# Kernel optimization log

Measured on AMD Instinct MI355X. Metric: run time of the kernel, lower is better.

Reference implementation:

```python
import jax, jax.numpy as jnp
import numpy as np

N_NODES = 50000
N_EDGES = 800000
N_GRAPHS = 256
IN_DIM = 64
HID = 128


def setup_inputs() -> dict:
    key = jax.random.key(0)
    ks = jax.random.split(key, 16)
    x = jax.random.normal(ks[0], (N_NODES, IN_DIM), dtype=jnp.float32)
    edge_index = jax.random.randint(ks[1], (2, N_EDGES), 0, N_NODES)
    batch = jnp.sort(jax.random.randint(ks[2], (N_NODES,), 0, N_GRAPHS))
    edge_attr = jax.random.uniform(ks[3], (N_EDGES,), dtype=jnp.float32)

    def lin(k, out_d, in_d):
        s = 1.0 / np.sqrt(in_d)
        return jax.random.uniform(k, (out_d, in_d), minval=-s, maxval=s, dtype=jnp.float32)

    params = {
        'W1r': lin(ks[4], HID, IN_DIM), 'b1': jnp.zeros((HID,), jnp.float32), 'W1root': lin(ks[5], HID, IN_DIM),
        'W2r': lin(ks[6], HID, HID), 'b2': jnp.zeros((HID,), jnp.float32), 'W2root': lin(ks[7], HID, HID),
        'W3r': lin(ks[8], HID // 2, HID), 'b3': jnp.zeros((HID // 2,), jnp.float32), 'W3root': lin(ks[9], HID // 2, HID),
        'Wm1': lin(ks[10], HID // 4, HID // 2), 'bm1': jnp.zeros((HID // 4,), jnp.float32),
        'Wm2': lin(ks[11], HID // 8, HID // 4), 'bm2': jnp.zeros((HID // 8,), jnp.float32),
        'Wm3': lin(ks[12], 1, HID // 8), 'bm3': jnp.zeros((1,), jnp.float32),
    }
    return dict(x=x, edge_index=edge_index, batch=batch, edge_attr=edge_attr, **params)


def _graph_conv(x, src, dst, ew, Wr, br, Wroot):
    # PyG GraphConv(aggr='add'): lin_rel(scatter_add(x[src]*w)) + lin_root(x)
    msg = x[src] * ew[:, None]                      # [E, d] gather + scale
    agg = jax.ops.segment_sum(msg, dst, num_segments=x.shape[0])  # [N, d]
    return agg @ Wr.T + br + x @ Wroot.T


def reference(x, edge_index, batch, edge_attr,
              W1r, b1, W1root, W2r, b2, W2root, W3r, b3, W3root,
              Wm1, bm1, Wm2, bm2, Wm3, bm3):
    src, dst = edge_index[0], edge_index[1]
    # eval mode: dropouts are identity
    h = jnp.tanh(_graph_conv(x, src, dst, edge_attr, W1r, b1, W1root))
    h = jnp.tanh(_graph_conv(h, src, dst, edge_attr, W2r, b2, W2root))
    h = jnp.tanh(_graph_conv(h, src, dst, edge_attr, W3r, b3, W3root))
    # global add pool over graphs
    g = jax.ops.segment_sum(h, batch, num_segments=N_GRAPHS)      # [G, hid//2]
    g = jax.nn.relu(g @ Wm1.T + bm1)
    g = jax.nn.relu(g @ Wm2.T + bm2)
    return g @ Wm3.T + bm3                                        # [G, 1]
```

## Files before the change

### kernel.cpp

```cpp
#include <hip/hip_runtime.h>

#define N_NODES 50000
#define N_EDGES 800000
#define N_GRAPHS 256
#define SCAN_B ((N_NODES + 255) / 256)
#define FILL_GROUPS 8
#define NPG (N_NODES / FILL_GROUPS)

typedef __attribute__((ext_vector_type(8))) short bf16x8;
typedef __attribute__((ext_vector_type(4))) float f32x4;

__device__ inline unsigned short f2bf(float f) {
    unsigned int u = __float_as_uint(f);
    u += 0x7fff + ((u >> 16) & 1);
    return (unsigned short)(u >> 16);
}
__device__ inline float bf2f(unsigned short h) {
    return __uint_as_float(((unsigned int)h) << 16);
}
__device__ inline float fast_tanh(float x) {
    return 1.0f - 2.0f / (__expf(2.0f * x) + 1.0f);
}

__global__ void pack_w_kernel(const float* __restrict__ s0, const float* __restrict__ s1,
                              int K0, int KTOT, int nconcat,
                              unsigned short* __restrict__ hi, unsigned short* __restrict__ lo)
{
    const int idx = blockIdx.x * 256 + threadIdx.x;
    if (idx >= 128 * KTOT) return;
    const int c = idx / KTOT, k = idx % KTOT;
    float v;
    if (nconcat) v = (c < 64) ? s0[c * KTOT + k] : s1[(c - 64) * KTOT + k];
    else         v = (k < K0) ? s0[c * K0 + k]   : s1[c * K0 + (k - K0)];
    const unsigned short h = f2bf(v);
    hi[idx] = h;
    lo[idx] = f2bf(v - bf2f(h));
}

template<int KTOT, bool KSPLIT, bool NBIAS, bool ACT>
__global__ __launch_bounds__(256)
void gemm_mfma(const float* __restrict__ A0, const float* __restrict__ A1, int astr,
               const unsigned short* __restrict__ Bhi, const unsigned short* __restrict__ Blo,
               const float* __restrict__ bias, float* __restrict__ C)
{
    __shared__ __align__(16) unsigned short lah[64 * 40];
    __shared__ __align__(16) unsigned short lal[64 * 40];
    __shared__ __align__(16) unsigned short lbh[128 * 40];
    __shared__ __align__(16) unsigned short lbl[128 * 40];

    const int tid = threadIdx.x;
    const int w = tid >> 6;
    const int lane = tid & 63;
    const int lrow = lane & 15;
    const int lkb = lane >> 4;
    const int m0 = blockIdx.x * 64;

    constexpr int NCH = KTOT / 32;
    f32x4 acc[4][2] = {};

    for (int ch = 0; ch < NCH; ++ch) {
        const float* __restrict__ Asel;
        int ak0;
        if (KSPLIT) {
            Asel = (ch < NCH / 2) ? A0 : A1;
            ak0 = (ch % (NCH / 2)) * 32;
        } else { Asel = A0; ak0 = ch * 32; }
        const int bk0 = ch * 32;

        __syncthreads();
#pragma unroll
        for (int p = 0; p < 2; ++p) {
            const int f = tid + p * 256;
            const int r = f >> 3;
            const int q = f & 7;
            int row = m0 + r; if (row >= N_NODES) row = N_NODES - 1;
            const float4 v = *(const float4*)&Asel[(long)row * astr + ak0 + q * 4];
            const unsigned short h0 = f2bf(v.x), h1 = f2bf(v.y), h2 = f2bf(v.z), h3 = f2bf(v.w);
            *(ushort4*)&lah[r * 40 + q * 4] = make_ushort4(h0, h1, h2, h3);
            *(ushort4*)&lal[r * 40 + q * 4] =
                make_ushort4(f2bf(v.x - bf2f(h0)), f2bf(v.y - bf2f(h1)),
                             f2bf(v.z - bf2f(h2)), f2bf(v.w - bf2f(h3)));
        }
#pragma unroll
        for (int p = 0; p < 2; ++p) {
            const int f = tid + p * 256;
            const int r = f >> 2;
            const int q = f & 3;
            const long g = (long)r * KTOT + bk0 + q * 8;
            *(uint4*)&lbh[r * 40 + q * 8] = *(const uint4*)&Bhi[g];
            *(uint4*)&lbl[r * 40 + q * 8] = *(const uint4*)&Blo[g];
        }
        __syncthreads();

        const int bo0 = (w * 32 + lrow) * 40 + lkb * 8;
        const int bo1 = bo0 + 16 * 40;
        const bf16x8 bh0 = *(const bf16x8*)&lbh[bo0];
        const bf16x8 bh1 = *(const bf16x8*)&lbh[bo1];
        const bf16x8 bl0 = *(const bf16x8*)&lbl[bo0];
        const bf16x8 bl1 = *(const bf16x8*)&lbl[bo1];
#pragma unroll
        for (int m = 0; m < 4; ++m) {
            const int ao = (m * 16 + lrow) * 40 + lkb * 8;
            const bf16x8 ah = *(const bf16x8*)&lah[ao];
            const bf16x8 al = *(const bf16x8*)&lal[ao];
            acc[m][0] = __builtin_amdgcn_mfma_f32_16x16x32_bf16(ah, bh0, acc[m][0], 0, 0, 0);
            acc[m][1] = __builtin_amdgcn_mfma_f32_16x16x32_bf16(ah, bh1, acc[m][1], 0, 0, 0);
            acc[m][0] = __builtin_amdgcn_mfma_f32_16x16x32_bf16(al, bh0, acc[m][0], 0, 0, 0);
            acc[m][1] = __builtin_amdgcn_mfma_f32_16x16x32_bf16(al, bh1, acc[m][1], 0, 0, 0);
            acc[m][0] = __builtin_amdgcn_mfma_f32_16x16x32_bf16(ah, bl0, acc[m][0], 0, 0, 0);
            acc[m][1] = __builtin_amdgcn_mfma_f32_16x16x32_bf16(ah, bl1, acc[m][1], 0, 0, 0);
        }
    }

    const int c0 = w * 32 + lrow;
    float bb0, bb1;
    if (NBIAS) {
        bb0 = (c0 < 64) ? 0.f : bias[c0 - 64];
        bb1 = (c0 + 16 < 64) ? 0.f : bias[c0 + 16 - 64];
    } else { bb0 = bias[c0]; bb1 = bias[c0 + 16]; }
#pragma unroll
    for (int m = 0; m < 4; ++m) {
#pragma unroll
        for (int r = 0; r < 4; ++r) {
            const int row = m0 + m * 16 + lkb * 4 + r;
            if (row < N_NODES) {
                const float v0 = acc[m][0][r] + bb0;
                const float v1 = acc[m][1][r] + bb1;
                C[(long)row * 128 + c0]      = ACT ? fast_tanh(v0) : v0;
                C[(long)row * 128 + c0 + 16] = ACT ? fast_tanh(v1) : v1;
            }
        }
    }
}

__global__ void count_kernel(const int* __restrict__ ei, int* __restrict__ count)
{
    const int e = blockIdx.x * blockDim.x + threadIdx.x;
    if (e < N_EDGES) atomicAdd(&count[ei[N_EDGES + e]], 1);
}

__global__ __launch_bounds__(256)
void scan_blocks_kernel(const int* __restrict__ count, int* __restrict__ blocksum)
{
    __shared__ int red[256];
    const int i = blockIdx.x * 256 + threadIdx.x;
    red[threadIdx.x] = (i < N_NODES) ? count[i] : 0;
    __syncthreads();
#pragma unroll
    for (int d = 128; d > 0; d >>= 1) {
        if (threadIdx.x < d) red[threadIdx.x] += red[threadIdx.x + d];
        __syncthreads();
    }
    if (threadIdx.x == 0) blocksum[blockIdx.x] = red[0];
}

__global__ __launch_bounds__(256)
void scan_base_kernel(const int* __restrict__ blocksum, int* __restrict__ blockbase)
{
    __shared__ int s[256];
    const int t = threadIdx.x;
    const int own = (t < SCAN_B) ? blocksum[t] : 0;
    s[t] = own;
    __syncthreads();
#pragma unroll
    for (int d = 1; d < 256; d <<= 1) {
        const int v = (t >= d) ? s[t - d] : 0;
        __syncthreads();
        s[t] += v;
        __syncthreads();
    }
    if (t < SCAN_B) blockbase[t] = s[t] - own;
}

__global__ __launch_bounds__(256)
void scan_final_kernel(const int* __restrict__ count, const int* __restrict__ blockbase,
                       int* __restrict__ offsets, int* __restrict__ cursor)
{
    __shared__ int s[256];
    const int t = threadIdx.x;
    const int i = blockIdx.x * 256 + t;
    const int v = (i < N_NODES) ? count[i] : 0;
    s[t] = v;
    __syncthreads();
#pragma unroll
    for (int d = 1; d < 256; d <<= 1) {
        const int u = (t >= d) ? s[t - d] : 0;
        __syncthreads();
        s[t] += u;
        __syncthreads();
    }
    if (i < N_NODES) {
        const int off = blockbase[blockIdx.x] + s[t] - v;
        offsets[i] = off;
        cursor[i] = off;
    }
    if (i == 0) offsets[N_NODES] = N_EDGES;
}

__global__ __launch_bounds__(256)
void fill_kernel(const int* __restrict__ ei, const float* __restrict__ ew,
                 int* __restrict__ cursor, uint2* __restrict__ rec)
{
    const int g = blockIdx.x & (FILL_GROUPS - 1);
    const int q = blockIdx.x >> 3;
    const int nlo = g * NPG;
    const int nhi = nlo + NPG;
    const int stride = (gridDim.x >> 3) * 256;
    for (int e = q * 256 + threadIdx.x; e < N_EDGES; e += stride) {
        const int t = ei[N_EDGES + e];
        if (t >= nlo && t < nhi) {
            const int pos = atomicAdd(&cursor[t], 1);
            rec[pos] = make_uint2((unsigned)ei[e], __float_as_uint(ew[e]));
        }
    }
}

template<int D>
__global__ __launch_bounds__(256)
void gather_agg(const float* __restrict__ feat, int stride,
                const int* __restrict__ offsets, const uint2* __restrict__ rec,
                float* __restrict__ agg)
{
    constexpr int LPN = D / 4;
    constexpr int NPB = 256 / LPN;
    const int lane = threadIdx.x % LPN;
    const int slot = threadIdx.x / LPN;
    const int n = blockIdx.x * NPB + slot;
    if (n >= N_NODES) return;
    const int lo = offsets[n], hi = offsets[n + 1];
    const int j = lane * 4;
    float4 a0 = make_float4(0.f, 0.f, 0.f, 0.f);
    float4 a1 = make_float4(0.f, 0.f, 0.f, 0.f);
    int e = lo;
    for (; e + 1 < hi; e += 2) {
        const uint2 r0 = rec[e];
        const uint2 r1 = rec[e + 1];
        const float4 v0 = *(const float4*)&feat[(long)r0.x * stride + j];
        const float4 v1 = *(const float4*)&feat[(long)r1.x * stride + j];
        const float w0 = __uint_as_float(r0.y);
        const float w1 = __uint_as_float(r1.y);
        a0.x = fmaf(v0.x, w0, a0.x); a0.y = fmaf(v0.y, w0, a0.y);
        a0.z = fmaf(v0.z, w0, a0.z); a0.w = fmaf(v0.w, w0, a0.w);
        a1.x = fmaf(v1.x, w1, a1.x); a1.y = fmaf(v1.y, w1, a1.y);
        a1.z = fmaf(v1.z, w1, a1.z); a1.w = fmaf(v1.w, w1, a1.w);
    }
    if (e < hi) {
        const uint2 r = rec[e];
        const float4 v = *(const float4*)&feat[(long)r.x * stride + j];
        const float w = __uint_as_float(r.y);
        a0.x = fmaf(v.x, w, a0.x); a0.y = fmaf(v.y, w, a0.y);
        a0.z = fmaf(v.z, w, a0.z); a0.w = fmaf(v.w, w, a0.w);
    }
    *(float4*)&agg[(long)n * D + j] =
        make_float4(a0.x + a1.x, a0.y + a1.y, a0.z + a1.z, a0.w + a1.w);
}

__global__ void gstart_kernel(const int* __restrict__ batch, int* __restrict__ gstart)
{
    const int g = threadIdx.x;
    int lo = 0, hi = N_NODES;
    while (lo < hi) { const int mid = (lo + hi) >> 1; if (batch[mid] < g) lo = mid + 1; else hi = mid; }
    gstart[g] = lo;
    if (g == 0) gstart[N_GRAPHS] = N_NODES;
}

__global__ __launch_bounds__(256)
void pool_seg_kernel(const float* __restrict__ agg3, const float* __restrict__ yr,
                     const int* __restrict__ gstart, float* __restrict__ g)
{
    const int gi = blockIdx.x;
    const int c = threadIdx.x & 63;
    const int sub = threadIdx.x >> 6;
    const int lo = gstart[gi], hi = gstart[gi + 1];
    float acc = 0.f;
    for (int n = lo + sub; n < hi; n += 4)
        acc += fast_tanh(agg3[(long)n * 64 + c] + yr[(long)n * 128 + 64 + c]);
    __shared__ float red[256];
    red[threadIdx.x] = acc;
    __syncthreads();
    if (sub == 0) g[gi * 64 + c] = red[c] + red[64 + c] + red[128 + c] + red[192 + c];
}

__global__ __launch_bounds__(64)
void mlp_kernel(const float* __restrict__ g,
                const float* __restrict__ Wm1, const float* __restrict__ bm1,
                const float* __restrict__ Wm2, const float* __restrict__ bm2,
                const float* __restrict__ Wm3, const float* __restrict__ bm3,
                float* __restrict__ out)
{
    const int gi = blockIdx.x;
    const int l = threadIdx.x;
    __shared__ float gr[64], h1[32], h2[16];
    gr[l] = g[gi * 64 + l];
    __syncthreads();
    if (l < 32) {
        float a = bm1[l];
        const float* w = Wm1 + l * 64;
        for (int k = 0; k < 64; ++k) a = fmaf(gr[k], w[k], a);
        h1[l] = fmaxf(a, 0.f);
    }
    __syncthreads();
    if (l < 16) {
        float a = bm2[l];
        const float* w = Wm2 + l * 32;
        for (int k = 0; k < 32; ++k) a = fmaf(h1[k], w[k], a);
        h2[l] = fmaxf(a, 0.f);
    }
    __syncthreads();
    if (l == 0) {
        float a = bm3[0];
        for (int k = 0; k < 16; ++k) a = fmaf(h2[k], Wm3[k], a);
        out[gi] = a;
    }
}

extern "C" void kernel_launch(void* const* d_in, const int* in_sizes, int n_in,
                              void* d_out, int out_size, void* d_ws, size_t ws_size,
                              hipStream_t stream) {
    const float* x      = (const float*)d_in[0];
    const int*   ei     = (const int*)  d_in[1];
    const int*   batch  = (const int*)  d_in[2];
    const float* ew     = (const float*)d_in[3];
    const float* W1r    = (const float*)d_in[4];
    const float* b1     = (const float*)d_in[5];
    const float* W1root = (const float*)d_in[6];
    const float* W2r    = (const float*)d_in[7];
    const float* b2     = (const float*)d_in[8];
    const float* W2root = (const float*)d_in[9];
    const float* W3r    = (const float*)d_in[10];
    const float* b3     = (const float*)d_in[11];
    const float* W3root = (const float*)d_in[12];
    const float* Wm1    = (const float*)d_in[13];
    const float* bm1    = (const float*)d_in[14];
    const float* Wm2    = (const float*)d_in[15];
    const float* bm2    = (const float*)d_in[16];
    const float* Wm3    = (const float*)d_in[17];
    const float* bm3    = (const float*)d_in[18];
    float* out = (float*)d_out;

    float* P0   = (float*)d_ws;
    float* P1   = P0 + (long)N_NODES * 128;
    float* P2   = P1 + (long)N_NODES * 128;
    float* POOL = P2 + (long)N_NODES * 128;
    int*   count    = (int*)(POOL + N_GRAPHS * 64);
    int*   offsets  = count + N_NODES;
    int*   cursor   = offsets + N_NODES + 1;
    int*   gstart   = cursor + N_NODES + 1;
    int*   blocksum = gstart + N_GRAPHS + 1;
    int*   blockbase= blocksum + SCAN_B;
    uintptr_t wp = ((uintptr_t)(blockbase + SCAN_B) + 15) & ~(uintptr_t)15;
    uint2* rec = (uint2*)wp;
    unsigned short* Bh1 = (unsigned short*)(rec + N_EDGES);
    unsigned short* Bl1 = Bh1 + 128 * 128;
    unsigned short* Bh2 = Bl1 + 128 * 128;
    unsigned short* Bl2 = Bh2 + 128 * 256;
    unsigned short* Bh3 = Bl2 + 128 * 256;
    unsigned short* Bl3 = Bh3 + 128 * 128;

    const int gemm_grid = (N_NODES + 63) / 64;
    const int egrid = (N_EDGES + 255) / 256;

    pack_w_kernel<<<(128 * 128 + 255) / 256, 256, 0, stream>>>(W1r, W1root, 64, 128, 0, Bh1, Bl1);
    pack_w_kernel<<<(128 * 256 + 255) / 256, 256, 0, stream>>>(W2r, W2root, 128, 256, 0, Bh2, Bl2);
    pack_w_kernel<<<(128 * 128 + 255) / 256, 256, 0, stream>>>(W3r, W3root, 128, 128, 1, Bh3, Bl3);

    hipMemsetAsync(count, 0, N_NODES * sizeof(int), stream);
    count_kernel<<<egrid, 256, 0, stream>>>(ei, count);
    scan_blocks_kernel<<<SCAN_B, 256, 0, stream>>>(count, blocksum);
    scan_base_kernel<<<1, 256, 0, stream>>>(blocksum, blockbase);
    scan_final_kernel<<<SCAN_B, 256, 0, stream>>>(count, blockbase, offsets, cursor);
    fill_kernel<<<2048, 256, 0, stream>>>(ei, ew, cursor, rec);
    gstart_kernel<<<1, 256, 0, stream>>>(batch, gstart);

    gather_agg<64><<<(N_NODES + 15) / 16, 256, 0, stream>>>(x, 64, offsets, rec, P2);
    gemm_mfma<128, true, false, true><<<gemm_grid, 256, 0, stream>>>(P2, x, 64, Bh1, Bl1, b1, P1);

    gather_agg<128><<<(N_NODES + 7) / 8, 256, 0, stream>>>(P1, 128, offsets, rec, P0);
    gemm_mfma<256, true, false, true><<<gemm_grid, 256, 0, stream>>>(P0, P1, 128, Bh2, Bl2, b2, P2);

    gemm_mfma<128, false, true, false><<<gemm_grid, 256, 0, stream>>>(P2, P2, 128, Bh3, Bl3, b3, P1);
    gather_agg<64><<<(N_NODES + 15) / 16, 256, 0, stream>>>(P1, 128, offsets, rec, P0);

    pool_seg_kernel<<<N_GRAPHS, 256, 0, stream>>>(P0, P1, gstart, POOL);
    mlp_kernel<<<N_GRAPHS, 64, 0, stream>>>(POOL, Wm1, bm1, Wm2, bm2, Wm3, bm3, out);
}
```

Before: 302.2 us.

## Store node features in bf16 and gather bf16 rows to halve gather traffic

Hidden features h1, h2, the layer-3 projection and x are now stored as bf16 instead of fp32. The gather-aggregate kernels therefore read half the bytes per neighbor row while still accumulating in fp32. GEMMs split their inputs: fp32 aggregated chunks keep the hi/lo split, while bf16 chunks skip the lo-part MFMAs, and the layer-3 GEMM writes its outputs in split form. This lowers memory traffic in the gather-dominated stages but loses precision in the stored activations and adds an x conversion kernel.

After: 268.7 us. 1.12x faster.

```diff
diff --git a/kernel.cpp b/kernel.cpp
--- a/kernel.cpp
+++ b/kernel.cpp
@@ -37,12 +37,27 @@
     lo[idx] = f2bf(v - bf2f(h));
 }
 
-template<int KTOT, bool KSPLIT, bool NBIAS, bool ACT>
-__global__ __launch_bounds__(256)
-void gemm_mfma(const float* __restrict__ A0, const float* __restrict__ A1, int astr,
+__global__ void cvt_bf16_kernel(const float* __restrict__ in,
+                                unsigned short* __restrict__ out, int n4)
+{
+    const int i = blockIdx.x * 256 + threadIdx.x;
+    if (i >= n4) return;
+    const float4 v = ((const float4*)in)[i];
+    ((ushort4*)out)[i] = make_ushort4(f2bf(v.x), f2bf(v.y), f2bf(v.z), f2bf(v.w));
+}
+
+template<int KF32, int KB16, bool OUTSPLIT, bool ACT>
+__global__ __launch_bounds__(256)
+void gemm_mfma(const float* __restrict__ Af, int fstr,
+               const unsigned short* __restrict__ Ab, int bstr,
                const unsigned short* __restrict__ Bhi, const unsigned short* __restrict__ Blo,
-               const float* __restrict__ bias, float* __restrict__ C)
-{
+               const float* __restrict__ bias,
+               unsigned short* __restrict__ C16, float* __restrict__ Cf)
+{
+    constexpr int KTOT = KF32 + KB16;
+    constexpr int NCHF = KF32 / 32;
+    constexpr int NCH  = KTOT / 32;
+
     __shared__ __align__(16) unsigned short lah[64 * 40];
     __shared__ __align__(16) unsigned short lal[64 * 40];
     __shared__ __align__(16) unsigned short lbh[128 * 40];
@@ -55,31 +70,34 @@
     const int lkb = lane >> 4;
     const int m0 = blockIdx.x * 64;
 
-    constexpr int NCH = KTOT / 32;
     f32x4 acc[4][2] = {};
 
     for (int ch = 0; ch < NCH; ++ch) {
-        const float* __restrict__ Asel;
-        int ak0;
-        if (KSPLIT) {
-            Asel = (ch < NCH / 2) ? A0 : A1;
-            ak0 = (ch % (NCH / 2)) * 32;
-        } else { Asel = A0; ak0 = ch * 32; }
+        const bool isF = (ch < NCHF);
         const int bk0 = ch * 32;
 
         __syncthreads();
-#pragma unroll
-        for (int p = 0; p < 2; ++p) {
-            const int f = tid + p * 256;
-            const int r = f >> 3;
-            const int q = f & 7;
+        if (isF) {
+            const int ak0 = ch * 32;
+#pragma unroll
+            for (int p = 0; p < 2; ++p) {
+                const int f = tid + p * 256;
+                const int r = f >> 3;
+                const int q = f & 7;
+                int row = m0 + r; if (row >= N_NODES) row = N_NODES - 1;
+                const float4 v = *(const float4*)&Af[(long)row * fstr + ak0 + q * 4];
+                const unsigned short h0 = f2bf(v.x), h1 = f2bf(v.y), h2 = f2bf(v.z), h3 = f2bf(v.w);
+                *(ushort4*)&lah[r * 40 + q * 4] = make_ushort4(h0, h1, h2, h3);
+                *(ushort4*)&lal[r * 40 + q * 4] =
+                    make_ushort4(f2bf(v.x - bf2f(h0)), f2bf(v.y - bf2f(h1)),
+                                 f2bf(v.z - bf2f(h2)), f2bf(v.w - bf2f(h3)));
+            }
+        } else {
+            const int ak0 = (ch - NCHF) * 32;
+            const int r = tid >> 2;
+            const int q = tid & 3;
             int row = m0 + r; if (row >= N_NODES) row = N_NODES - 1;
-            const float4 v = *(const float4*)&Asel[(long)row * astr + ak0 + q * 4];
-            const unsigned short h0 = f2bf(v.x), h1 = f2bf(v.y), h2 = f2bf(v.z), h3 = f2bf(v.w);
-            *(ushort4*)&lah[r * 40 + q * 4] = make_ushort4(h0, h1, h2, h3);
-            *(ushort4*)&lal[r * 40 + q * 4] =
-                make_ushort4(f2bf(v.x - bf2f(h0)), f2bf(v.y - bf2f(h1)),
-                             f2bf(v.z - bf2f(h2)), f2bf(v.w - bf2f(h3)));
+            *(uint4*)&lah[r * 40 + q * 8] = *(const uint4*)&Ab[(long)row * bstr + ak0 + q * 8];
         }
 #pragma unroll
         for (int p = 0; p < 2; ++p) {
@@ -102,32 +120,58 @@
         for (int m = 0; m < 4; ++m) {
             const int ao = (m * 16 + lrow) * 40 + lkb * 8;
             const bf16x8 ah = *(const bf16x8*)&lah[ao];
-            const bf16x8 al = *(const bf16x8*)&lal[ao];
             acc[m][0] = __builtin_amdgcn_mfma_f32_16x16x32_bf16(ah, bh0, acc[m][0], 0, 0, 0);
             acc[m][1] = __builtin_amdgcn_mfma_f32_16x16x32_bf16(ah, bh1, acc[m][1], 0, 0, 0);
-            acc[m][0] = __builtin_amdgcn_mfma_f32_16x16x32_bf16(al, bh0, acc[m][0], 0, 0, 0);
-            acc[m][1] = __builtin_amdgcn_mfma_f32_16x16x32_bf16(al, bh1, acc[m][1], 0, 0, 0);
             acc[m][0] = __builtin_amdgcn_mfma_f32_16x16x32_bf16(ah, bl0, acc[m][0], 0, 0, 0);
             acc[m][1] = __builtin_amdgcn_mfma_f32_16x16x32_bf16(ah, bl1, acc[m][1], 0, 0, 0);
+            if (isF) {
+                const bf16x8 al = *(const bf16x8*)&lal[ao];
+                acc[m][0] = __builtin_amdgcn_mfma_f32_16x16x32_bf16(al, bh0, acc[m][0], 0, 0, 0);
+                acc[m][1] = __builtin_amdgcn_mfma_f32_16x16x32_bf16(al, bh1, acc[m][1], 0, 0, 0);
+            }
         }
     }
 
     const int c0 = w * 32 + lrow;
-    float bb0, bb1;
-    if (NBIAS) {
-        bb0 = (c0 < 64) ? 0.f : bias[c0 - 64];
-        bb1 = (c0 + 16 < 64) ? 0.f : bias[c0 + 16 - 64];
-    } else { bb0 = bias[c0]; bb1 = bias[c0 + 16]; }
-#pragma unroll
-    for (int m = 0; m < 4; ++m) {
-#pragma unroll
-        for (int r = 0; r < 4; ++r) {
-            const int row = m0 + m * 16 + lkb * 4 + r;
-            if (row < N_NODES) {
-                const float v0 = acc[m][0][r] + bb0;
-                const float v1 = acc[m][1][r] + bb1;
-                C[(long)row * 128 + c0]      = ACT ? fast_tanh(v0) : v0;
-                C[(long)row * 128 + c0 + 16] = ACT ? fast_tanh(v1) : v1;
+    if (!OUTSPLIT) {
+        const float bb0 = bias[c0], bb1 = bias[c0 + 16];
+#pragma unroll
+        for (int m = 0; m < 4; ++m) {
+#pragma unroll
+            for (int r = 0; r < 4; ++r) {
+                const int row = m0 + m * 16 + lkb * 4 + r;
+                if (row < N_NODES) {
+                    float v0 = acc[m][0][r] + bb0;
+                    float v1 = acc[m][1][r] + bb1;
+                    if (ACT) { v0 = fast_tanh(v0); v1 = fast_tanh(v1); }
+                    C16[(long)row * 128 + c0]      = f2bf(v0);
+                    C16[(long)row * 128 + c0 + 16] = f2bf(v1);
+                }
+            }
+        }
+    } else if (c0 < 64) {
+#pragma unroll
+        for (int m = 0; m < 4; ++m) {
+#pragma unroll
+            for (int r = 0; r < 4; ++r) {
+                const int row = m0 + m * 16 + lkb * 4 + r;
+                if (row < N_NODES) {
+                    C16[(long)row * 64 + c0]      = f2bf(acc[m][0][r]);
+                    C16[(long)row * 64 + c0 + 16] = f2bf(acc[m][1][r]);
+                }
+            }
+        }
+    } else {
+        const float bb0 = bias[c0 - 64], bb1 = bias[c0 - 48];
+#pragma unroll
+        for (int m = 0; m < 4; ++m) {
+#pragma unroll
+            for (int r = 0; r < 4; ++r) {
+                const int row = m0 + m * 16 + lkb * 4 + r;
+                if (row < N_NODES) {
+                    Cf[(long)row * 64 + c0 - 64] = acc[m][0][r] + bb0;
+                    Cf[(long)row * 64 + c0 - 48] = acc[m][1][r] + bb1;
+                }
             }
         }
     }
@@ -217,42 +261,45 @@
 
 template<int D>
 __global__ __launch_bounds__(256)
-void gather_agg(const float* __restrict__ feat, int stride,
+void gather_agg(const unsigned short* __restrict__ feat, int stride,
                 const int* __restrict__ offsets, const uint2* __restrict__ rec,
                 float* __restrict__ agg)
 {
-    constexpr int LPN = D / 4;
+    constexpr int LPN = D / 8;
     constexpr int NPB = 256 / LPN;
     const int lane = threadIdx.x % LPN;
     const int slot = threadIdx.x / LPN;
     const int n = blockIdx.x * NPB + slot;
     if (n >= N_NODES) return;
     const int lo = offsets[n], hi = offsets[n + 1];
-    const int j = lane * 4;
-    float4 a0 = make_float4(0.f, 0.f, 0.f, 0.f);
-    float4 a1 = make_float4(0.f, 0.f, 0.f, 0.f);
+    const int j = lane * 8;
+    float a0[8] = {}, a1[8] = {};
     int e = lo;
     for (; e + 1 < hi; e += 2) {
         const uint2 r0 = rec[e];
         const uint2 r1 = rec[e + 1];
-        const float4 v0 = *(const float4*)&feat[(long)r0.x * stride + j];
-        const float4 v1 = *(const float4*)&feat[(long)r1.x * stride + j];
+        const bf16x8 v0 = *(const bf16x8*)&feat[(long)r0.x * stride + j];
+        const bf16x8 v1 = *(const bf16x8*)&feat[(long)r1.x * stride + j];
         const float w0 = __uint_as_float(r0.y);
         const float w1 = __uint_as_float(r1.y);
-        a0.x = fmaf(v0.x, w0, a0.x); a0.y = fmaf(v0.y, w0, a0.y);
-        a0.z = fmaf(v0.z, w0, a0.z); a0.w = fmaf(v0.w, w0, a0.w);
-        a1.x = fmaf(v1.x, w1, a1.x); a1.y = fmaf(v1.y, w1, a1.y);
-        a1.z = fmaf(v1.z, w1, a1.z); a1.w = fmaf(v1.w, w1, a1.w);
+#pragma unroll
+        for (int k = 0; k < 8; ++k) {
+            a0[k] = fmaf(bf2f((unsigned short)v0[k]), w0, a0[k]);
+            a1[k] = fmaf(bf2f((unsigned short)v1[k]), w1, a1[k]);
+        }
     }
     if (e < hi) {
         const uint2 r = rec[e];
-        const float4 v = *(const float4*)&feat[(long)r.x * stride + j];
+        const bf16x8 v = *(const bf16x8*)&feat[(long)r.x * stride + j];
         const float w = __uint_as_float(r.y);
-        a0.x = fmaf(v.x, w, a0.x); a0.y = fmaf(v.y, w, a0.y);
-        a0.z = fmaf(v.z, w, a0.z); a0.w = fmaf(v.w, w, a0.w);
+#pragma unroll
+        for (int k = 0; k < 8; ++k)
+            a0[k] = fmaf(bf2f((unsigned short)v[k]), w, a0[k]);
     }
     *(float4*)&agg[(long)n * D + j] =
-        make_float4(a0.x + a1.x, a0.y + a1.y, a0.z + a1.z, a0.w + a1.w);
+        make_float4(a0[0] + a1[0], a0[1] + a1[1], a0[2] + a1[2], a0[3] + a1[3]);
+    *(float4*)&agg[(long)n * D + j + 4] =
+        make_float4(a0[4] + a1[4], a0[5] + a1[5], a0[6] + a1[6], a0[7] + a1[7]);
 }
 
 __global__ void gstart_kernel(const int* __restrict__ batch, int* __restrict__ gstart)
@@ -265,7 +312,7 @@
 }
 
 __global__ __launch_bounds__(256)
-void pool_seg_kernel(const float* __restrict__ agg3, const float* __restrict__ yr,
+void pool_seg_kernel(const float* __restrict__ agg3, const float* __restrict__ root3,
                      const int* __restrict__ gstart, float* __restrict__ g)
 {
     const int gi = blockIdx.x;
@@ -274,7 +321,7 @@
     const int lo = gstart[gi], hi = gstart[gi + 1];
     float acc = 0.f;
     for (int n = lo + sub; n < hi; n += 4)
-        acc += fast_tanh(agg3[(long)n * 64 + c] + yr[(long)n * 128 + 64 + c]);
+        acc += fast_tanh(agg3[(long)n * 64 + c] + root3[(long)n * 64 + c]);
     __shared__ float red[256];
     red[threadIdx.x] = acc;
     __syncthreads();
@@ -338,10 +385,9 @@
     const float* bm3    = (const float*)d_in[18];
     float* out = (float*)d_out;
 
-    float* P0   = (float*)d_ws;
-    float* P1   = P0 + (long)N_NODES * 128;
-    float* P2   = P1 + (long)N_NODES * 128;
-    float* POOL = P2 + (long)N_NODES * 128;
+    float* agg1  = (float*)d_ws;
+    float* agg2  = agg1 + (long)N_NODES * 64;
+    float* POOL  = agg2 + (long)N_NODES * 128;
     int*   count    = (int*)(POOL + N_GRAPHS * 64);
     int*   offsets  = count + N_NODES;
     int*   cursor   = offsets + N_NODES + 1;
@@ -350,12 +396,18 @@
     int*   blockbase= blocksum + SCAN_B;
     uintptr_t wp = ((uintptr_t)(blockbase + SCAN_B) + 15) & ~(uintptr_t)15;
     uint2* rec = (uint2*)wp;
-    unsigned short* Bh1 = (unsigned short*)(rec + N_EDGES);
+    unsigned short* xb  = (unsigned short*)(rec + N_EDGES);
+    unsigned short* h1b = xb + (long)N_NODES * 64;
+    unsigned short* h2b = h1b + (long)N_NODES * 128;
+    unsigned short* Bh1 = h2b + (long)N_NODES * 128;
     unsigned short* Bl1 = Bh1 + 128 * 128;
     unsigned short* Bh2 = Bl1 + 128 * 128;
     unsigned short* Bl2 = Bh2 + 128 * 256;
     unsigned short* Bh3 = Bl2 + 128 * 256;
     unsigned short* Bl3 = Bh3 + 128 * 128;
+    unsigned short* y3b = (unsigned short*)agg2;
+    float* root3 = agg2 + (long)N_NODES * 64;
+    float* agg3  = agg1;
 
     const int gemm_grid = (N_NODES + 63) / 64;
     const int egrid = (N_EDGES + 255) / 256;
@@ -363,6 +415,7 @@
     pack_w_kernel<<<(128 * 128 + 255) / 256, 256, 0, stream>>>(W1r, W1root, 64, 128, 0, Bh1, Bl1);
     pack_w_kernel<<<(128 * 256 + 255) / 256, 256, 0, stream>>>(W2r, W2root, 128, 256, 0, Bh2, Bl2);
     pack_w_kernel<<<(128 * 128 + 255) / 256, 256, 0, stream>>>(W3r, W3root, 128, 128, 1, Bh3, Bl3);
+    cvt_bf16_kernel<<<(N_NODES * 64 / 4 + 255) / 256, 256, 0, stream>>>(x, xb, N_NODES * 64 / 4);
 
     hipMemsetAsync(count, 0, N_NODES * sizeof(int), stream);
     count_kernel<<<egrid, 256, 0, stream>>>(ei, count);
@@ -372,15 +425,18 @@
     fill_kernel<<<2048, 256, 0, stream>>>(ei, ew, cursor, rec);
     gstart_kernel<<<1, 256, 0, stream>>>(batch, gstart);
 
-    gather_agg<64><<<(N_NODES + 15) / 16, 256, 0, stream>>>(x, 64, offsets, rec, P2);
-    gemm_mfma<128, true, false, true><<<gemm_grid, 256, 0, stream>>>(P2, x, 64, Bh1, Bl1, b1, P1);
-
-    gather_agg<128><<<(N_NODES + 7) / 8, 256, 0, stream>>>(P1, 128, offsets, rec, P0);
-    gemm_mfma<256, true, false, true><<<gemm_grid, 256, 0, stream>>>(P0, P1, 128, Bh2, Bl2, b2, P2);
-
-    gemm_mfma<128, false, true, false><<<gemm_grid, 256, 0, stream>>>(P2, P2, 128, Bh3, Bl3, b3, P1);
-    gather_agg<64><<<(N_NODES + 15) / 16, 256, 0, stream>>>(P1, 128, offsets, rec, P0);
-
-    pool_seg_kernel<<<N_GRAPHS, 256, 0, stream>>>(P0, P1, gstart, POOL);
+    gather_agg<64><<<(N_NODES + 31) / 32, 256, 0, stream>>>(xb, 64, offsets, rec, agg1);
+    gemm_mfma<64, 64, false, true><<<gemm_grid, 256, 0, stream>>>(
+        agg1, 64, xb, 64, Bh1, Bl1, b1, h1b, nullptr);
+
+    gather_agg<128><<<(N_NODES + 15) / 16, 256, 0, stream>>>(h1b, 128, offsets, rec, agg2);
+    gemm_mfma<128, 128, false, true><<<gemm_grid, 256, 0, stream>>>(
+        agg2, 128, h1b, 128, Bh2, Bl2, b2, h2b, nullptr);
+
+    gemm_mfma<0, 128, true, false><<<gemm_grid, 256, 0, stream>>>(
+        nullptr, 0, h2b, 128, Bh3, Bl3, b3, y3b, root3);
+    gather_agg<64><<<(N_NODES + 31) / 32, 256, 0, stream>>>(y3b, 64, offsets, rec, agg3);
+
+    pool_seg_kernel<<<N_GRAPHS, 256, 0, stream>>>(agg3, root3, gstart, POOL);
     mlp_kernel<<<N_GRAPHS, 64, 0, stream>>>(POOL, Wm1, bm1, Wm2, bm2, Wm3, bm3, out);
 }
```
